# Optimization experiments

Hardware: AMD Instinct MI355X
Metric: run time of the kernel (lower is better)

The kernel has to match this reference:

```python
import jax, jax.numpy as jnp
import numpy as np

N = 100000   # input nodes
M = 100000   # output nodes (size = (N, M))
NNZ = 3_200_000  # edges, avg_degree 32
B = 32       # batch
D = 32       # Kaiming channel dim


def setup_inputs() -> dict:
    key = jax.random.key(0)
    k1, k2, k3 = jax.random.split(key, 3)
    # COO indices: row 0 = src (in [0, N)), row 1 = dst (in [0, M))
    indices = jax.random.randint(k1, (2, NNZ), 0, N, dtype=jnp.int32)
    # Kaiming init: randn * sqrt(2/d), as in the torch module when d is given
    values = jax.random.normal(k2, (NNZ,), dtype=jnp.float32) * np.float32((2.0 / D) ** 0.5)
    bias = jnp.zeros((M, 1), dtype=jnp.float32)
    x = jax.random.normal(k3, (B, N, 1), dtype=jnp.float32)
    return {"x": x, "indices": indices, "values": values, "bias": bias}


def reference(x, indices, values, bias):
    # Equivalent of: for each b, sparse.mm(W.T, x[b]) + bias, W in COO (N, M)
    # y[b, m] = sum_{e: dst[e]==m} values[e] * x[b, src[e]] + bias[m]
    src = indices[0]
    dst = indices[1]
    contrib = x[:, src, 0] * values[None, :]           # (B, NNZ) gather-multiply
    y = jax.ops.segment_sum(contrib.T, dst, num_segments=M)  # (M, B) scatter-add
    return (y.T + bias[:, 0][None, :])[..., None]       # (B, M, 1)
```

## Files before the change

### kernel.cpp

```cpp
#include <hip/hip_runtime.h>
#include <hip/hip_fp16.h>
#include <stdint.h>

#define NB 32
#define BIN_SHIFT 6
#define BIN_ROWS 64
#define NBINS_MAX 2048
#define CSHIFT 10
#define NC_MAX 128
#define FPC 16
#define FCHUNK 8192
#define FTHREADS 1024
#define EPT (FCHUNK / FTHREADS)
#define CAP_C 34816
#define P2CHUNK 8192
#define CH2 ((CAP_C + P2CHUNK - 1) / P2CHUNK)
#define EPT2 (P2CHUNK / FTHREADS)
#define SRC_BITS 18
#define SRC_MASK ((1u << SRC_BITS) - 1)
#define CAP 2816
#define MAXK 11


__global__ void transpose_x_kernel(const float* __restrict__ x,
                                   __half* __restrict__ xt, int N) {
    __shared__ float tile[32][33];
    int n0 = blockIdx.x * 32;
    for (int i = threadIdx.y; i < 32; i += 8) {
        int n = n0 + threadIdx.x;
        tile[i][threadIdx.x] = (n < N) ? x[(size_t)i * N + n] : 0.f;
    }
    __syncthreads();
    for (int i = threadIdx.y; i < 32; i += 8) {
        int n = n0 + i;
        if (n < N) xt[(size_t)n * NB + threadIdx.x] =
            __float2half(tile[threadIdx.x][i]);
    }
}

__global__ void fill_coarse(const int* __restrict__ src,
                            const int* __restrict__ dst,
                            const float* __restrict__ vals,
                            int* __restrict__ cCursor,
                            uint2* __restrict__ cCsr,
                            int* __restrict__ fineCnt,
                            int* __restrict__ ovCount,
                            int* __restrict__ ovList,
                            int nnz, int ncoarse, int nbins) {
    __shared__ int lhist[NC_MAX];
    __shared__ int lbase[NC_MAX];
    __shared__ int fh[NBINS_MAX];
    int t = threadIdx.x;
    int e0 = blockIdx.x * FCHUNK;
    int dcache[EPT];
    for (int i = t; i < NC_MAX; i += FTHREADS) lhist[i] = 0;
    for (int i = t; i < nbins; i += FTHREADS) fh[i] = 0;
    __syncthreads();
#pragma unroll
    for (int q = 0; q < EPT; ++q) {
        int e = e0 + q * FTHREADS + t;
        int d = (e < nnz) ? dst[e] : -1;
        dcache[q] = d;
        if (d >= 0) atomicAdd(&lhist[d >> CSHIFT], 1);
    }
    __syncthreads();
    for (int i = t; i < ncoarse; i += FTHREADS) {
        int c = lhist[i];
        lbase[i] = c ? atomicAdd(&cCursor[i], c) : 0;
        lhist[i] = 0;
    }
    __syncthreads();
#pragma unroll
    for (int q = 0; q < EPT; ++q) {
        int e = e0 + q * FTHREADS + t;
        int d = dcache[q];
        if (d >= 0) {
            int c = d >> CSHIFT;
            int r = lbase[c] + atomicAdd(&lhist[c], 1);
            if (r < CAP_C) {
                uint32_t meta = ((uint32_t)(d & 1023) << SRC_BITS) |
                                (uint32_t)src[e];
                cCsr[(size_t)c * CAP_C + r] =
                    make_uint2(meta, __float_as_uint(vals[e]));
                atomicAdd(&fh[d >> BIN_SHIFT], 1);
            } else {
                int op = atomicAdd(ovCount, 1);
                ovList[op] = e;
            }
        }
    }
    __syncthreads();
    for (int i = t; i < nbins; i += FTHREADS)
        if (fh[i]) atomicAdd(&fineCnt[i], fh[i]);
}

__global__ void fine_scan(const int* __restrict__ fineCnt,
                          int* __restrict__ fineBase,
                          int* __restrict__ fineCursor, int nbins) {
    __shared__ int s[1024];
    int t = threadIdx.x;
    int i0 = t * 2, i1 = t * 2 + 1;
    int v0 = (i0 < nbins) ? fineCnt[i0] : 0;
    int v1 = (i1 < nbins) ? fineCnt[i1] : 0;
    int sum = v0 + v1;
    s[t] = sum;
    __syncthreads();
    for (int off = 1; off < 1024; off <<= 1) {
        int add = (t >= off) ? s[t - off] : 0;
        __syncthreads();
        s[t] += add;
        __syncthreads();
    }
    int run = s[t] - sum;
    if (i0 < nbins) { fineBase[i0] = run; fineCursor[i0] = run; }
    run += v0;
    if (i1 < nbins) { fineBase[i1] = run; fineCursor[i1] = run; }
}

__global__ void fill_fine(const int* __restrict__ cCursor,
                          const uint2* __restrict__ cCsr,
                          int* __restrict__ fineCursor,
                          uint2* __restrict__ fineCsr) {
    __shared__ int lhist[FPC];
    __shared__ int lbase[FPC];
    int c = blockIdx.x / CH2;
    int i = blockIdx.x % CH2;
    int n  = min(cCursor[c], CAP_C);
    int j0 = i * P2CHUNK;
    int jn = min(j0 + P2CHUNK, n);
    if (j0 >= jn) return;
    int t = threadIdx.x;
    uint2 ecache[EPT2];
    if (t < FPC) lhist[t] = 0;
    __syncthreads();
    const uint2* reg = cCsr + (size_t)c * CAP_C;
#pragma unroll
    for (int q = 0; q < EPT2; ++q) {
        int j = j0 + q * FTHREADS + t;
        if (j < jn) {
            uint2 e = reg[j];
            ecache[q] = e;
            atomicAdd(&lhist[(e.x >> 24) & 15], 1);
        }
    }
    __syncthreads();
    if (t < FPC) {
        int cn = lhist[t];
        lbase[t] = cn ? atomicAdd(&fineCursor[c * FPC + t], cn) : 0;
        lhist[t] = 0;
    }
    __syncthreads();
#pragma unroll
    for (int q = 0; q < EPT2; ++q) {
        int j = j0 + q * FTHREADS + t;
        if (j < jn) {
            uint2 e = ecache[q];
            int f = (e.x >> 24) & 15;
            int p = lbase[f] + atomicAdd(&lhist[f], 1);
            fineCsr[p] = e;
        }
    }
}

__global__ __launch_bounds__(256) void sort_gather(
        const int* __restrict__ fineBase,
        const int* __restrict__ fineCursor,
        const uint2* __restrict__ csr,
        const __half* __restrict__ xt,
        const float* __restrict__ bias,
        float* __restrict__ out, int M) {
    __shared__ uint2 sorted[CAP];
    __shared__ int rowCnt[BIN_ROWS];
    __shared__ int rowOff[BIN_ROWS];
    int t = threadIdx.x;
    int bin = blockIdx.x;
    int start = fineBase[bin];
    int cnt   = fineCursor[bin] - start;
    int g = t >> 5;
    int b = t & 31;

    if (cnt <= CAP) {
        uint2 reg[MAXK];
#pragma unroll
        for (int k = 0; k < MAXK; ++k) {
            int j = t + k * 256;
            if (j < cnt) reg[k] = csr[start + j];
        }
        if (t < BIN_ROWS) rowCnt[t] = 0;
        __syncthreads();
#pragma unroll
        for (int k = 0; k < MAXK; ++k) {
            int j = t + k * 256;
            if (j < cnt)
                atomicAdd(&rowCnt[(reg[k].x >> SRC_BITS) & 63], 1);
        }
        __syncthreads();
        if (t == 0) {
            int run = 0;
#pragma unroll
            for (int r = 0; r < BIN_ROWS; ++r) {
                rowOff[r] = run;
                run += rowCnt[r];
            }
        }
        __syncthreads();
#pragma unroll
        for (int k = 0; k < MAXK; ++k) {
            int j = t + k * 256;
            if (j < cnt) {
                int p = atomicAdd(&rowOff[(reg[k].x >> SRC_BITS) & 63], 1);
                sorted[p] = reg[k];
            }
        }
        __syncthreads();
        for (int r = g; r < BIN_ROWS; r += 8) {
            int m = bin * BIN_ROWS + r;
            if (m >= M) break;
            int jend = rowOff[r];
            int jj   = jend - rowCnt[r];
            float acc0 = 0.f, acc1 = 0.f;
            for (; jj + 8 <= jend; jj += 8) {
                uint2 e0 = sorted[jj + 0];
                uint2 e1 = sorted[jj + 1];
                uint2 e2 = sorted[jj + 2];
                uint2 e3 = sorted[jj + 3];
                uint2 e4 = sorted[jj + 4];
                uint2 e5 = sorted[jj + 5];
                uint2 e6 = sorted[jj + 6];
                uint2 e7 = sorted[jj + 7];
                float x0 = __half2float(xt[(size_t)(e0.x & SRC_MASK) * NB + b]);
                float x1 = __half2float(xt[(size_t)(e1.x & SRC_MASK) * NB + b]);
                float x2 = __half2float(xt[(size_t)(e2.x & SRC_MASK) * NB + b]);
                float x3 = __half2float(xt[(size_t)(e3.x & SRC_MASK) * NB + b]);
                float x4 = __half2float(xt[(size_t)(e4.x & SRC_MASK) * NB + b]);
                float x5 = __half2float(xt[(size_t)(e5.x & SRC_MASK) * NB + b]);
                float x6 = __half2float(xt[(size_t)(e6.x & SRC_MASK) * NB + b]);
                float x7 = __half2float(xt[(size_t)(e7.x & SRC_MASK) * NB + b]);
                acc0 = fmaf(__uint_as_float(e0.y), x0, acc0);
                acc1 = fmaf(__uint_as_float(e1.y), x1, acc1);
                acc0 = fmaf(__uint_as_float(e2.y), x2, acc0);
                acc1 = fmaf(__uint_as_float(e3.y), x3, acc1);
                acc0 = fmaf(__uint_as_float(e4.y), x4, acc0);
                acc1 = fmaf(__uint_as_float(e5.y), x5, acc1);
                acc0 = fmaf(__uint_as_float(e6.y), x6, acc0);
                acc1 = fmaf(__uint_as_float(e7.y), x7, acc1);
            }
            for (; jj < jend; ++jj) {
                uint2 e = sorted[jj];
                acc0 = fmaf(__uint_as_float(e.y),
                            __half2float(xt[(size_t)(e.x & SRC_MASK) * NB + b]),
                            acc0);
            }
            out[(size_t)b * M + m] = acc0 + acc1 + bias[m];
        }
    } else {
        float* tile = (float*)sorted;
        for (int i = t; i < BIN_ROWS * NB; i += 256) tile[i] = 0.f;
        __syncthreads();
        for (int j = start + g; j < start + cnt; j += 8) {
            uint2 e = csr[j];
            float xv = __half2float(xt[(size_t)(e.x & SRC_MASK) * NB + b]);
            atomicAdd(&tile[((e.x >> SRC_BITS) & 63) * NB + b],
                      __uint_as_float(e.y) * xv);
        }
        __syncthreads();
        for (int i = t; i < BIN_ROWS * NB; i += 256) {
            int m = bin * BIN_ROWS + (i >> 5);
            if (m < M) out[(size_t)(i & 31) * M + m] = tile[i] + bias[m];
        }
    }
}

__global__ void fixup_kernel(const int* __restrict__ ovCount,
                             const int* __restrict__ ovList,
                             const int* __restrict__ src,
                             const int* __restrict__ dst,
                             const float* __restrict__ vals,
                             const __half* __restrict__ xt,
                             float* __restrict__ out, int M) {
    long long total = (long long)(*ovCount) * 32;
    long long stride = (long long)gridDim.x * blockDim.x;
    for (long long i = (long long)blockIdx.x * blockDim.x + threadIdx.x;
         i < total; i += stride) {
        int k = (int)(i >> 5);
        int b = (int)(i & 31);
        int e = ovList[k];
        atomicAdd(&out[(size_t)b * M + dst[e]],
                  vals[e] * __half2float(xt[(size_t)src[e] * NB + b]));
    }
}

__global__ void finalize_kernel(const float* __restrict__ yt,
                                const float* __restrict__ bias,
                                float* __restrict__ out, int M) {
    __shared__ float tile[32][33];
    int m0 = blockIdx.x * 32;
    for (int i = threadIdx.y; i < 32; i += 8) {
        int m = m0 + i;
        tile[i][threadIdx.x] = (m < M) ? yt[(size_t)m * NB + threadIdx.x] : 0.f;
    }
    __syncthreads();
    for (int i = threadIdx.y; i < 32; i += 8) {
        int m = m0 + threadIdx.x;
        if (m < M) out[(size_t)i * M + m] = tile[threadIdx.x][i] + bias[m];
    }
}

__global__ void scatter_kernel(const int* __restrict__ src,
                               const int* __restrict__ dst,
                               const float* __restrict__ vals,
                               const __half* __restrict__ xt,
                               float* __restrict__ yt, int nnz) {
    long long tid = (long long)blockIdx.x * blockDim.x + threadIdx.x;
    int e = (int)(tid >> 5);
    if (e >= nnz) return;
    int b = (int)(tid & 31);
    atomicAdd(&yt[(size_t)dst[e] * NB + b],
              vals[e] * __half2float(xt[(size_t)src[e] * NB + b]));
}

extern "C" void kernel_launch(void* const* d_in, const int* in_sizes, int n_in,
                              void* d_out, int out_size, void* d_ws, size_t ws_size,
                              hipStream_t stream) {
    const float* x       = (const float*)d_in[0];
    const int*   indices = (const int*)  d_in[1];
    const float* vals    = (const float*)d_in[2];
    const float* bias    = (const float*)d_in[3];

    float* out = (float*)d_out;

    int nnz = in_sizes[1] / 2;
    int N   = in_sizes[0] / NB;
    int M   = in_sizes[3];

    const int* src = indices;
    const int* dst = indices + nnz;

    int nbins   = (M + BIN_ROWS - 1) >> BIN_SHIFT;
    int ncoarse = (M + (1 << CSHIFT) - 1) >> CSHIFT;

    __half* xt         = (__half*)d_ws;
    int*    fineCnt    = (int*)(xt + (size_t)N * NB);
    int*    cCursor    = fineCnt + NBINS_MAX;
    int*    ovCount    = cCursor + NC_MAX;
    int*    fineBase   = ovCount + 4;
    int*    fineCursor = fineBase + NBINS_MAX;
    int*    ovList     = fineCursor + NBINS_MAX;
    uint2*  cCsr       = (uint2*)(((uintptr_t)(ovList + nnz) + 15) &
                                  ~(uintptr_t)15);
    uint2*  fineCsr    = cCsr + (size_t)ncoarse * CAP_C;

    size_t need = (size_t)((char*)(fineCsr + nnz) - (char*)d_ws);

    float* yt = (float*)(xt + (size_t)N * NB);
    size_t need_fb = (size_t)((char*)(yt + (size_t)M * NB) - (char*)d_ws);

    transpose_x_kernel<<<(N + 31) / 32, dim3(32, 8), 0, stream>>>(x, xt, N);

    if (ws_size >= need && nbins <= NBINS_MAX && ncoarse <= NC_MAX) {
        hipMemsetAsync(fineCnt, 0, (NBINS_MAX + NC_MAX + 4) * sizeof(int),
                       stream);
        int fgrid = (nnz + FCHUNK - 1) / FCHUNK;
        fill_coarse<<<fgrid, FTHREADS, 0, stream>>>(src, dst, vals, cCursor,
                                                    cCsr, fineCnt, ovCount,
                                                    ovList, nnz, ncoarse,
                                                    nbins);
        fine_scan<<<1, 1024, 0, stream>>>(fineCnt, fineBase, fineCursor,
                                          nbins);
        fill_fine<<<ncoarse * CH2, FTHREADS, 0, stream>>>(cCursor, cCsr,
                                                          fineCursor, fineCsr);
        sort_gather<<<nbins, 256, 0, stream>>>(fineBase, fineCursor, fineCsr,
                                               xt, bias, out, M);
        fixup_kernel<<<32, 256, 0, stream>>>(ovCount, ovList, src, dst, vals,
                                             xt, out, M);
    } else if (ws_size >= need_fb) {
        hipMemsetAsync(yt, 0, (size_t)M * NB * sizeof(float), stream);
        long long pairs = (long long)nnz * NB;
        int grid = (int)((pairs + 255) / 256);
        scatter_kernel<<<grid, 256, 0, stream>>>(src, dst, vals, xt, yt, nnz);
        finalize_kernel<<<(M + 31) / 32, dim3(32, 8), 0, stream>>>(yt, bias,
                                                                   out, M);
    }
}
```

Measured before the change: 198.1 us.

## Halve bin size to 32 rows and use per-wave histograms in fine fill

Shrinks the output-row bins from 64 to 32 rows, so there are twice as many bins, FPC becomes 32, and the per-bin shared-memory capacity and register caching (CAP, MAXK) are halved. The goal is more, smaller sort_gather blocks for better occupancy and load balance, with less shared-memory use per block. fill_fine now keeps a histogram per wavefront and computes per-wave offsets, which spreads out contention on the shared atomics. fine_scan handles 4 bins per thread to cover up to 4096 bins. The risks are that the bit layout of the packed meta field (shift 23 with mask 31) must match the encoding done in the unseen code, and that bins overflowing the smaller CAP fall back to the slower atomic path more often.

```diff
diff --git a/kernel.cpp b/kernel.cpp
--- a/kernel.cpp
+++ b/kernel.cpp
@@ -3,14 +3,15 @@
 #include <stdint.h>
 
 #define NB 32
-#define BIN_SHIFT 6
-#define BIN_ROWS 64
-#define NBINS_MAX 2048
+#define BIN_SHIFT 5
+#define BIN_ROWS 32
+#define NBINS_MAX 4096
 #define CSHIFT 10
 #define NC_MAX 128
-#define FPC 16
+#define FPC 32
 #define FCHUNK 8192
 #define FTHREADS 1024
+#define NWAVE (FTHREADS / 64)
 #define EPT (FCHUNK / FTHREADS)
 #define CAP_C 34816
 #define P2CHUNK 8192
@@ -18,8 +19,8 @@
 #define EPT2 (P2CHUNK / FTHREADS)
 #define SRC_BITS 18
 #define SRC_MASK ((1u << SRC_BITS) - 1)
-#define CAP 2816
-#define MAXK 11
+#define CAP 1408
+#define MAXK 6
 
 
 __global__ void transpose_x_kernel(const float* __restrict__ x,
@@ -99,10 +100,14 @@
                           int* __restrict__ fineCursor, int nbins) {
     __shared__ int s[1024];
     int t = threadIdx.x;
-    int i0 = t * 2, i1 = t * 2 + 1;
-    int v0 = (i0 < nbins) ? fineCnt[i0] : 0;
-    int v1 = (i1 < nbins) ? fineCnt[i1] : 0;
-    int sum = v0 + v1;
+    int v[4];
+    int sum = 0;
+#pragma unroll
+    for (int k = 0; k < 4; ++k) {
+        int i = t * 4 + k;
+        v[k] = (i < nbins) ? fineCnt[i] : 0;
+        sum += v[k];
+    }
     s[t] = sum;
     __syncthreads();
     for (int off = 1; off < 1024; off <<= 1) {
@@ -112,17 +117,19 @@
         __syncthreads();
     }
     int run = s[t] - sum;
-    if (i0 < nbins) { fineBase[i0] = run; fineCursor[i0] = run; }
-    run += v0;
-    if (i1 < nbins) { fineBase[i1] = run; fineCursor[i1] = run; }
+#pragma unroll
+    for (int k = 0; k < 4; ++k) {
+        int i = t * 4 + k;
+        if (i < nbins) { fineBase[i] = run; fineCursor[i] = run; }
+        run += v[k];
+    }
 }
 
 __global__ void fill_fine(const int* __restrict__ cCursor,
                           const uint2* __restrict__ cCsr,
                           int* __restrict__ fineCursor,
                           uint2* __restrict__ fineCsr) {
-    __shared__ int lhist[FPC];
-    __shared__ int lbase[FPC];
+    __shared__ int whist[NWAVE][FPC];
     int c = blockIdx.x / CH2;
     int i = blockIdx.x % CH2;
     int n  = min(cCursor[c], CAP_C);
@@ -130,8 +137,10 @@
     int jn = min(j0 + P2CHUNK, n);
     if (j0 >= jn) return;
     int t = threadIdx.x;
+    int w = t >> 6;
     uint2 ecache[EPT2];
-    if (t < FPC) lhist[t] = 0;
+    int* wflat = &whist[0][0];
+    if (t < NWAVE * FPC) wflat[t] = 0;
     __syncthreads();
     const uint2* reg = cCsr + (size_t)c * CAP_C;
 #pragma unroll
@@ -140,14 +149,22 @@
         if (j < jn) {
             uint2 e = reg[j];
             ecache[q] = e;
-            atomicAdd(&lhist[(e.x >> 24) & 15], 1);
+            atomicAdd(&whist[w][(e.x >> 23) & 31], 1);
         }
     }
     __syncthreads();
     if (t < FPC) {
-        int cn = lhist[t];
-        lbase[t] = cn ? atomicAdd(&fineCursor[c * FPC + t], cn) : 0;
-        lhist[t] = 0;
+        int total = 0;
+#pragma unroll
+        for (int w2 = 0; w2 < NWAVE; ++w2) total += whist[w2][t];
+        int base = total ? atomicAdd(&fineCursor[c * FPC + t], total) : 0;
+        int run = base;
+#pragma unroll
+        for (int w2 = 0; w2 < NWAVE; ++w2) {
+            int cn = whist[w2][t];
+            whist[w2][t] = run;
+            run += cn;
+        }
     }
     __syncthreads();
 #pragma unroll
@@ -155,8 +172,7 @@
         int j = j0 + q * FTHREADS + t;
         if (j < jn) {
             uint2 e = ecache[q];
-            int f = (e.x >> 24) & 15;
-            int p = lbase[f] + atomicAdd(&lhist[f], 1);
+            int p = atomicAdd(&whist[w][(e.x >> 23) & 31], 1);
             fineCsr[p] = e;
         }
     }
@@ -192,7 +208,7 @@
         for (int k = 0; k < MAXK; ++k) {
             int j = t + k * 256;
             if (j < cnt)
-                atomicAdd(&rowCnt[(reg[k].x >> SRC_BITS) & 63], 1);
+                atomicAdd(&rowCnt[(reg[k].x >> SRC_BITS) & 31], 1);
         }
         __syncthreads();
         if (t == 0) {
@@ -208,7 +224,7 @@
         for (int k = 0; k < MAXK; ++k) {
             int j = t + k * 256;
             if (j < cnt) {
-                int p = atomicAdd(&rowOff[(reg[k].x >> SRC_BITS) & 63], 1);
+                int p = atomicAdd(&rowOff[(reg[k].x >> SRC_BITS) & 31], 1);
                 sorted[p] = reg[k];
             }
         }
@@ -260,7 +276,7 @@
         for (int j = start + g; j < start + cnt; j += 8) {
             uint2 e = csr[j];
             float xv = __half2float(xt[(size_t)(e.x & SRC_MASK) * NB + b]);
-            atomicAdd(&tile[((e.x >> SRC_BITS) & 63) * NB + b],
+            atomicAdd(&tile[((e.x >> SRC_BITS) & 31) * NB + b],
                       __uint_as_float(e.y) * xv);
         }
         __syncthreads();
```

Measured after the change: 203.3 us. 2.6% more time.
